# Performance work log

Measured on AMD Instinct MI355X. Metric: run time of the kernel, lower is better.

## Reference

```python
import jax, jax.numpy as jnp
import numpy as np

NUM_BINS = 30
MIN_BW = 1e-3
MIN_BH = 1e-3
MIN_D = 1e-3
LO_IN, HI_IN = 0.0, 1.0
LO_OUT, HI_OUT = 0.0, 1.0
DERIV_OUT_LO = (HI_OUT - LO_OUT) / (HI_IN - LO_IN)  # default outside derivatives
DERIV_OUT_HI = DERIV_OUT_LO
EPS = 1e-6
B, V = 65536, 64


def _cumparams(unnorm, lo, hi, min_size):
    # softmax bin sizes with a floor, cumsum into knot positions. [V,K] -> ([V,K+1],[V,K])
    K = unnorm.shape[-1]
    p = jax.nn.softmax(unnorm, axis=-1)
    p = min_size + (1.0 - min_size * K) * p
    cp = jnp.cumsum(p, axis=-1)
    cp = jnp.pad(cp, [(0, 0), (1, 0)])
    cp = (hi - lo) * cp + lo
    cp = cp.at[..., 0].set(lo).at[..., -1].set(hi)
    sizes = cp[..., 1:] - cp[..., :-1]
    return cp, sizes


def setup_inputs() -> dict:
    key = jax.random.key(0)
    k0, k1, k2, k3 = jax.random.split(key, 4)
    return {
        "inputs": jax.random.uniform(k0, (B, V), dtype=jnp.float32),
        "unnormalized_widths": jax.random.uniform(k1, (V, NUM_BINS), dtype=jnp.float32),
        "unnormalized_heights": jax.random.uniform(k2, (V, NUM_BINS), dtype=jnp.float32),
        "unnormalized_derivatives": jax.random.uniform(k3, (V, NUM_BINS - 1), dtype=jnp.float32),
    }


def reference(inputs, unnormalized_widths, unnormalized_heights, unnormalized_derivatives):
    K = NUM_BINS
    nb, nv = inputs.shape

    cumw, widths = _cumparams(unnormalized_widths, LO_IN, HI_IN, MIN_BW)      # [V,K+1],[V,K]
    cumh, heights = _cumparams(unnormalized_heights, LO_OUT, HI_OUT, MIN_BH)  # [V,K+1],[V,K]

    # boundary derivatives pinned so softplus(const)+MIN_D == 1
    const = float(np.log(np.exp(1.0 - MIN_D) - 1.0))
    ud = jnp.pad(unnormalized_derivatives, [(0, 0), (1, 1)], constant_values=const)
    derivs = MIN_D + jax.nn.softplus(ud)  # [V,K+1]
    delta = heights / widths              # [V,K]

    # per-element bin search (forward mode -> search in cumwidths)
    bounds = cumw.at[..., -1].add(EPS)                                   # [V,K+1]
    bin_idx = jnp.sum(inputs[..., None] >= bounds[None], axis=-1) - 1    # [B,V]
    bin_idx = jnp.clip(bin_idx, 0, K - 1)

    vidx = jnp.arange(nv)[None, :]  # broadcast variable index [1,V]
    icw = cumw[vidx, bin_idx]       # input_cumwidths [B,V]
    ibw = widths[vidx, bin_idx]
    ich = cumh[vidx, bin_idx]
    idl = delta[vidx, bin_idx]
    d0 = derivs[vidx, bin_idx]
    d1 = derivs[vidx, bin_idx + 1]
    ih = heights[vidx, bin_idx]

    theta = (inputs - icw) / ibw
    t1mt = theta * (1.0 - theta)
    numerator = ih * (idl * theta * theta + d0 * t1mt)
    denominator = idl + (d0 + d1 - 2.0 * idl) * t1mt
    spline_out = ich + numerator / denominator
    deriv_num = idl * idl * (d1 * theta * theta + 2.0 * idl * t1mt + d0 * (1.0 - theta) ** 2)
    spline_lad = jnp.log(deriv_num) - 2.0 * jnp.log(denominator)

    below = inputs < LO_IN
    above = inputs > HI_IN
    inside = ~(below | above)
    out_lo = LO_OUT + (inputs - LO_IN) * DERIV_OUT_LO
    out_hi = HI_OUT + (inputs - HI_IN) * DERIV_OUT_HI
    outputs = jnp.where(below, out_lo, jnp.where(above, out_hi, spline_out))
    logabsdet = jnp.where(inside, spline_lad, 0.0)
    return outputs, logabsdet
```

## Files before the change

kernel.cpp:

```cpp
#include <hip/hip_runtime.h>
#include <math.h>


#define NB 65536
#define NV 64
#define NKB 30
#define ROWF 153
#define OFF_B 0
#define OFF_W 32
#define OFF_C 62
#define OFF_H 92
#define OFF_D 122
#define NBLK 1024

__global__ __launch_bounds__(64) void rqs_params(const float* __restrict__ uw,
                                                 const float* __restrict__ uh,
                                                 const float* __restrict__ ud,
                                                 float* __restrict__ P) {
  const int v = blockIdx.x;
  const int lane = threadIdx.x;
  float* p = P + v * ROWF;
  const float MINB = 1e-3f;
  const float scale = 1.0f - MINB * (float)NKB;

  {
    float u = (lane < NKB) ? uw[v * NKB + lane] : -1e30f;
    float m = u;
#pragma unroll
    for (int s = 32; s >= 1; s >>= 1) m = fmaxf(m, __shfl_xor(m, s));
    float e = (lane < NKB) ? expf(u - m) : 0.0f;
    float t = e;
#pragma unroll
    for (int s = 32; s >= 1; s >>= 1) t += __shfl_xor(t, s);
    float pk = (lane < NKB) ? (MINB + scale * (e / t)) : 0.0f;
    float ci = pk;
#pragma unroll
    for (int s = 1; s < 64; s <<= 1) {
      float z = __shfl_up(ci, s);
      if (lane >= s) ci += z;
    }
    float ce = ci - pk;
    float nxt = (lane == NKB - 1) ? 1.0f : ci;
    if (lane < NKB) {
      p[OFF_B + lane + 1] = nxt;
      p[OFF_W + lane] = 1.0f / (nxt - ce);
    }
    if (lane == 0) p[OFF_B + 0] = 0.0f;
    if (lane == NKB) p[OFF_B + NKB] = 1.0f + 1e-6f;
    if (lane == NKB + 1) p[OFF_B + NKB + 1] = 3.0e38f;
  }
  {
    float u = (lane < NKB) ? uh[v * NKB + lane] : -1e30f;
    float m = u;
#pragma unroll
    for (int s = 32; s >= 1; s >>= 1) m = fmaxf(m, __shfl_xor(m, s));
    float e = (lane < NKB) ? expf(u - m) : 0.0f;
    float t = e;
#pragma unroll
    for (int s = 32; s >= 1; s >>= 1) t += __shfl_xor(t, s);
    float pk = (lane < NKB) ? (MINB + scale * (e / t)) : 0.0f;
    float ci = pk;
#pragma unroll
    for (int s = 1; s < 64; s <<= 1) {
      float z = __shfl_up(ci, s);
      if (lane >= s) ci += z;
    }
    float ce = ci - pk;
    float nxt = (lane == NKB - 1) ? 1.0f : ci;
    if (lane < NKB) {
      p[OFF_C + lane] = ce;
      p[OFF_H + lane] = nxt - ce;
    }
  }
  {
    const float CST = (float)log(exp(1.0 - 1e-3) - 1.0);
    if (lane <= NKB) {
      float x = (lane == 0 || lane == NKB) ? CST : ud[v * (NKB - 1) + lane - 1];
      float sp = (x > 0.f) ? (x + log1pf(expf(-x))) : log1pf(expf(x));
      p[OFF_D + lane] = 1e-3f + sp;
    }
  }
}

__global__ __launch_bounds__(256, 4) void rqs_main(const float* __restrict__ x,
                                                   const float* __restrict__ P,
                                                   float* __restrict__ out) {
  __shared__ float lds[NV * ROWF];
  {
    const float4* src = (const float4*)P;
    float4* dst = (float4*)lds;
    for (int i = threadIdx.x; i < (NV * ROWF) / 4; i += 256) dst[i] = src[i];
  }
  __syncthreads();

  const int N = NB * NV;
  const int n4 = N / 4;
  for (int gid = blockIdx.x * 256 + threadIdx.x; gid < n4; gid += NBLK * 256) {
    float4 xv = ((const float4*)x)[gid];
    int v0 = (gid & 15) * 4;

    float xs[4] = {xv.x, xv.y, xv.z, xv.w};
    float o[4], l[4];
#pragma unroll
    for (int j = 0; j < 4; ++j) {
      float xx = xs[j];
      const float* row = lds + (v0 + j) * ROWF;
      int idx = 0;
#pragma unroll
      for (int s = 16; s >= 1; s >>= 1) {
        int c = idx + s;
        idx = (xx >= row[OFF_B + c]) ? c : idx;
      }
      int b = idx > 29 ? 29 : idx;

      float icw  = row[OFF_B + b];
      float winv = row[OFF_W + b];
      float ich  = row[OFF_C + b];
      float ih   = row[OFF_H + b];
      float d0   = row[OFF_D + b];
      float d1   = row[OFF_D + b + 1];
      float idl  = ih * winv;

      float th   = (xx - icw) * winv;
      float omt  = 1.0f - th;
      float t1mt = th * omt;
      float th2  = th * th;
      float num  = ih * (idl * th2 + d0 * t1mt);
      float den  = idl + (d0 + d1 - 2.0f * idl) * t1mt;
      float rden = __frcp_rn(den);
      float so   = ich + num * rden;
      float dn   = idl * idl * (d1 * th2 + 2.0f * idl * t1mt + d0 * omt * omt);
      float sl   = __logf(dn * rden * rden);

      bool inside = !(xx < 0.0f) && !(xx > 1.0f);
      o[j] = inside ? so : xx;
      l[j] = inside ? sl : 0.0f;
    }
    float4 ov = {o[0], o[1], o[2], o[3]};
    float4 lv = {l[0], l[1], l[2], l[3]};
    ((float4*)out)[gid] = ov;
    ((float4*)(out + N))[gid] = lv;
  }
}

extern "C" void kernel_launch(void* const* d_in, const int* in_sizes, int n_in,
                              void* d_out, int out_size, void* d_ws, size_t ws_size,
                              hipStream_t stream) {
  const float* x  = (const float*)d_in[0];
  const float* uw = (const float*)d_in[1];
  const float* uh = (const float*)d_in[2];
  const float* ud = (const float*)d_in[3];
  float* out = (float*)d_out;
  float* P   = (float*)d_ws;

  rqs_params<<<NV, 64, 0, stream>>>(uw, uh, ud, P);
  rqs_main<<<NBLK, 256, 0, stream>>>(x, P, out);
}
```

Baseline: 92.01 us.

## Fuse parameter kernel into main kernel, recomputing spline tables per block in LDS

Drops the separate parameter-precompute kernel and its global workspace round trip. Each block now computes the softmax/cumsum/softplus tables for all 64 variables itself, with each of its 4 waves handling 16 variables, and writes them straight into shared memory. This removes one kernel launch and the dependency between the two kernels. In exchange, every one of the 1024 blocks repeats the table computation serially, which adds transcendental work and shuffle latency to each block's prologue.

After: 125.2 us. 36.0% more time.

```diff
diff --git a/kernel.cpp b/kernel.cpp
--- a/kernel.cpp
+++ b/kernel.cpp
@@ -13,83 +13,76 @@
 #define OFF_D 122
 #define NBLK 1024
 
-__global__ __launch_bounds__(64) void rqs_params(const float* __restrict__ uw,
-                                                 const float* __restrict__ uh,
-                                                 const float* __restrict__ ud,
-                                                 float* __restrict__ P) {
-  const int v = blockIdx.x;
-  const int lane = threadIdx.x;
-  float* p = P + v * ROWF;
+__global__ __launch_bounds__(256, 4) void rqs_fused(const float* __restrict__ x,
+                                                    const float* __restrict__ uw,
+                                                    const float* __restrict__ uh,
+                                                    const float* __restrict__ ud,
+                                                    float* __restrict__ out) {
+  __shared__ float lds[NV * ROWF];
+  const int lane = threadIdx.x & 63;
+  const int wave = threadIdx.x >> 6;
   const float MINB = 1e-3f;
   const float scale = 1.0f - MINB * (float)NKB;
 
-  {
-    float u = (lane < NKB) ? uw[v * NKB + lane] : -1e30f;
-    float m = u;
+  for (int t = 0; t < 16; ++t) {
+    const int v = wave * 16 + t;
+    float* p = lds + v * ROWF;
+
+    {
+      float u = (lane < NKB) ? uw[v * NKB + lane] : -1e30f;
+      float m = u;
 #pragma unroll
-    for (int s = 32; s >= 1; s >>= 1) m = fmaxf(m, __shfl_xor(m, s));
-    float e = (lane < NKB) ? expf(u - m) : 0.0f;
-    float t = e;
+      for (int s = 32; s >= 1; s >>= 1) m = fmaxf(m, __shfl_xor(m, s));
+      float e = (lane < NKB) ? expf(u - m) : 0.0f;
+      float tt = e;
 #pragma unroll
-    for (int s = 32; s >= 1; s >>= 1) t += __shfl_xor(t, s);
-    float pk = (lane < NKB) ? (MINB + scale * (e / t)) : 0.0f;
-    float ci = pk;
+      for (int s = 32; s >= 1; s >>= 1) tt += __shfl_xor(tt, s);
+      float pk = (lane < NKB) ? (MINB + scale * (e / tt)) : 0.0f;
+      float ci = pk;
 #pragma unroll
-    for (int s = 1; s < 64; s <<= 1) {
-      float z = __shfl_up(ci, s);
-      if (lane >= s) ci += z;
+      for (int s = 1; s < 64; s <<= 1) {
+        float z = __shfl_up(ci, s);
+        if (lane >= s) ci += z;
+      }
+      float ce = ci - pk;
+      float nxt = (lane == NKB - 1) ? 1.0f : ci;
+      if (lane < NKB - 1) p[OFF_B + lane + 1] = nxt;
+      if (lane < NKB) p[OFF_W + lane] = 1.0f / (nxt - ce);
+      if (lane == 0) p[OFF_B + 0] = 0.0f;
+      if (lane == NKB) p[OFF_B + NKB] = 1.0f + 1e-6f;
+      if (lane == NKB + 1) p[OFF_B + NKB + 1] = 3.0e38f;
     }
-    float ce = ci - pk;
-    float nxt = (lane == NKB - 1) ? 1.0f : ci;
-    if (lane < NKB) {
-      p[OFF_B + lane + 1] = nxt;
-      p[OFF_W + lane] = 1.0f / (nxt - ce);
+    {
+      float u = (lane < NKB) ? uh[v * NKB + lane] : -1e30f;
+      float m = u;
+#pragma unroll
+      for (int s = 32; s >= 1; s >>= 1) m = fmaxf(m, __shfl_xor(m, s));
+      float e = (lane < NKB) ? expf(u - m) : 0.0f;
+      float tt = e;
+#pragma unroll
+      for (int s = 32; s >= 1; s >>= 1) tt += __shfl_xor(tt, s);
+      float pk = (lane < NKB) ? (MINB + scale * (e / tt)) : 0.0f;
+      float ci = pk;
+#pragma unroll
+      for (int s = 1; s < 64; s <<= 1) {
+        float z = __shfl_up(ci, s);
+        if (lane >= s) ci += z;
+      }
+      float ce = ci - pk;
+      float nxt = (lane == NKB - 1) ? 1.0f : ci;
+      if (lane < NKB) {
+        p[OFF_C + lane] = ce;
+        p[OFF_H + lane] = nxt - ce;
+      }
     }
-    if (lane == 0) p[OFF_B + 0] = 0.0f;
-    if (lane == NKB) p[OFF_B + NKB] = 1.0f + 1e-6f;
-    if (lane == NKB + 1) p[OFF_B + NKB + 1] = 3.0e38f;
-  }
-  {
-    float u = (lane < NKB) ? uh[v * NKB + lane] : -1e30f;
-    float m = u;
-#pragma unroll
-    for (int s = 32; s >= 1; s >>= 1) m = fmaxf(m, __shfl_xor(m, s));
-    float e = (lane < NKB) ? expf(u - m) : 0.0f;
-    float t = e;
-#pragma unroll
-    for (int s = 32; s >= 1; s >>= 1) t += __shfl_xor(t, s);
-    float pk = (lane < NKB) ? (MINB + scale * (e / t)) : 0.0f;
-    float ci = pk;
-#pragma unroll
-    for (int s = 1; s < 64; s <<= 1) {
-      float z = __shfl_up(ci, s);
-      if (lane >= s) ci += z;
+    {
+      const float CST = (float)log(exp(1.0 - 1e-3) - 1.0);
+      if (lane <= NKB) {
+        float xv = (lane == 0 || lane == NKB) ? CST : ud[v * (NKB - 1) + lane - 1];
+        float sp = (xv > 0.f) ? (xv + log1pf(expf(-xv))) : log1pf(expf(xv));
+        p[OFF_D + lane] = 1e-3f + sp;
+      }
     }
-    float ce = ci - pk;
-    float nxt = (lane == NKB - 1) ? 1.0f : ci;
-    if (lane < NKB) {
-      p[OFF_C + lane] = ce;
-      p[OFF_H + lane] = nxt - ce;
-    }
-  }
-  {
-    const float CST = (float)log(exp(1.0 - 1e-3) - 1.0);
-    if (lane <= NKB) {
-      float x = (lane == 0 || lane == NKB) ? CST : ud[v * (NKB - 1) + lane - 1];
-      float sp = (x > 0.f) ? (x + log1pf(expf(-x))) : log1pf(expf(x));
-      p[OFF_D + lane] = 1e-3f + sp;
-    }
-  }
-}
-
-__global__ __launch_bounds__(256, 4) void rqs_main(const float* __restrict__ x,
-                                                   const float* __restrict__ P,
-                                                   float* __restrict__ out) {
-  __shared__ float lds[NV * ROWF];
-  {
-    const float4* src = (const float4*)P;
-    float4* dst = (float4*)lds;
-    for (int i = threadIdx.x; i < (NV * ROWF) / 4; i += 256) dst[i] = src[i];
   }
   __syncthreads();
 
@@ -151,8 +144,6 @@
   const float* uh = (const float*)d_in[2];
   const float* ud = (const float*)d_in[3];
   float* out = (float*)d_out;
-  float* P   = (float*)d_ws;
 
-  rqs_params<<<NV, 64, 0, stream>>>(uw, uh, ud, P);
-  rqs_main<<<NBLK, 256, 0, stream>>>(x, P, out);
+  rqs_fused<<<NBLK, 256, 0, stream>>>(x, uw, uh, ud, out);
 }
```

## Replace dependent binary bin search with two-level parallel count search

Applied to the files above, without the earlier changes.

Replaces the 5-step dependent binary search over knot positions with a two-level search. It loads 7 coarse knots per element, counts how many are exceeded to pick a group of 4, then loads 3 fine knots and counts again. Loads are batched across the 4 elements so LDS latency overlaps instead of chaining. It also swaps the correctly rounded reciprocal for the raw hardware rcp, and the params kernel stops writing knot 30 from lane 29 (lane 30 writes it instead). The change does more LDS reads per element in exchange for fewer serial load-compare steps, and may raise register pressure.

After: 93.29 us. No clear change (+1.4%).

```diff
diff --git a/kernel.cpp b/kernel.cpp
--- a/kernel.cpp
+++ b/kernel.cpp
@@ -41,10 +41,8 @@
     }
     float ce = ci - pk;
     float nxt = (lane == NKB - 1) ? 1.0f : ci;
-    if (lane < NKB) {
-      p[OFF_B + lane + 1] = nxt;
-      p[OFF_W + lane] = 1.0f / (nxt - ce);
-    }
+    if (lane < NKB - 1) p[OFF_B + lane + 1] = nxt;
+    if (lane < NKB) p[OFF_W + lane] = 1.0f / (nxt - ce);
     if (lane == 0) p[OFF_B + 0] = 0.0f;
     if (lane == NKB) p[OFF_B + NKB] = 1.0f + 1e-6f;
     if (lane == NKB + 1) p[OFF_B + NKB + 1] = 3.0e38f;
@@ -97,41 +95,66 @@
   const int n4 = N / 4;
   for (int gid = blockIdx.x * 256 + threadIdx.x; gid < n4; gid += NBLK * 256) {
     float4 xv = ((const float4*)x)[gid];
-    int v0 = (gid & 15) * 4;
+    const int v0 = (gid & 15) * 4;
+    float xs[4] = {xv.x, xv.y, xv.z, xv.w};
+    const float* rows[4];
+#pragma unroll
+    for (int j = 0; j < 4; ++j) rows[j] = lds + (v0 + j) * ROWF;
 
-    float xs[4] = {xv.x, xv.y, xv.z, xv.w};
+    float pA[4][7];
+#pragma unroll
+    for (int j = 0; j < 4; ++j)
+#pragma unroll
+      for (int i = 0; i < 7; ++i) pA[j][i] = rows[j][OFF_B + 4 * (i + 1)];
+    int base[4];
+#pragma unroll
+    for (int j = 0; j < 4; ++j) {
+      int c = 0;
+#pragma unroll
+      for (int i = 0; i < 7; ++i) c += (xs[j] >= pA[j][i]) ? 4 : 0;
+      base[j] = c;
+    }
+    float pB[4][3];
+#pragma unroll
+    for (int j = 0; j < 4; ++j)
+#pragma unroll
+      for (int t = 0; t < 3; ++t) pB[j][t] = rows[j][OFF_B + base[j] + t + 1];
+    int bb[4];
+#pragma unroll
+    for (int j = 0; j < 4; ++j) {
+      int m = 0;
+#pragma unroll
+      for (int t = 0; t < 3; ++t) m += (xs[j] >= pB[j][t]) ? 1 : 0;
+      int b = base[j] + m;
+      bb[j] = b > 29 ? 29 : b;
+    }
+    float icw[4], winv[4], ich[4], ih[4], d0[4], d1[4];
+#pragma unroll
+    for (int j = 0; j < 4; ++j) {
+      const float* r = rows[j];
+      const int b = bb[j];
+      icw[j]  = r[OFF_B + b];
+      winv[j] = r[OFF_W + b];
+      ich[j]  = r[OFF_C + b];
+      ih[j]   = r[OFF_H + b];
+      d0[j]   = r[OFF_D + b];
+      d1[j]   = r[OFF_D + b + 1];
+    }
     float o[4], l[4];
 #pragma unroll
     for (int j = 0; j < 4; ++j) {
-      float xx = xs[j];
-      const float* row = lds + (v0 + j) * ROWF;
-      int idx = 0;
-#pragma unroll
-      for (int s = 16; s >= 1; s >>= 1) {
-        int c = idx + s;
-        idx = (xx >= row[OFF_B + c]) ? c : idx;
-      }
-      int b = idx > 29 ? 29 : idx;
-
-      float icw  = row[OFF_B + b];
-      float winv = row[OFF_W + b];
-      float ich  = row[OFF_C + b];
-      float ih   = row[OFF_H + b];
-      float d0   = row[OFF_D + b];
-      float d1   = row[OFF_D + b + 1];
-      float idl  = ih * winv;
-
-      float th   = (xx - icw) * winv;
+      float xx   = xs[j];
+      float idl  = ih[j] * winv[j];
+      float th   = (xx - icw[j]) * winv[j];
       float omt  = 1.0f - th;
       float t1mt = th * omt;
       float th2  = th * th;
-      float num  = ih * (idl * th2 + d0 * t1mt);
-      float den  = idl + (d0 + d1 - 2.0f * idl) * t1mt;
-      float rden = __frcp_rn(den);
-      float so   = ich + num * rden;
-      float dn   = idl * idl * (d1 * th2 + 2.0f * idl * t1mt + d0 * omt * omt);
+      float num  = ih[j] * (idl * th2 + d0[j] * t1mt);
+      float den  = idl + (d0[j] + d1[j] - 2.0f * idl) * t1mt;
+      float rden = __builtin_amdgcn_rcpf(den);
+      float so   = ich[j] + num * rden;
+      float dn   = idl * idl * (d1[j] * th2 + 2.0f * idl * t1mt + d0[j] * omt * omt);
       float sl   = __logf(dn * rden * rden);
-
       bool inside = !(xx < 0.0f) && !(xx > 1.0f);
       o[j] = inside ? so : xx;
       l[j] = inside ? sl : 0.0f;
```

## Use 512-thread blocks with two prefetched float4 loads per thread

Applied to the files above, without the earlier changes.

Raises the block size to 512 and replaces the grid-stride loop with a fixed two-iteration body. Both input float4 loads are issued up front, before any compute, to raise memory-level parallelism. The reciprocal changes from round-to-nearest to the hardware rcp builtin. The params kernel also stops writing the last knot from the cumsum, because that slot is overwritten by the pinned boundary value. Together these cut loop overhead and aim to hide global load latency, at the cost of hardcoding the grid to cover exactly N/4 elements in two passes.

Result: no change. 90.87 us (-1.2%).

```diff
diff --git a/kernel.cpp b/kernel.cpp
--- a/kernel.cpp
+++ b/kernel.cpp
@@ -12,6 +12,7 @@
 #define OFF_H 92
 #define OFF_D 122
 #define NBLK 1024
+#define BSZ 512
 
 __global__ __launch_bounds__(64) void rqs_params(const float* __restrict__ uw,
                                                  const float* __restrict__ uh,
@@ -41,10 +42,8 @@
     }
     float ce = ci - pk;
     float nxt = (lane == NKB - 1) ? 1.0f : ci;
-    if (lane < NKB) {
-      p[OFF_B + lane + 1] = nxt;
-      p[OFF_W + lane] = 1.0f / (nxt - ce);
-    }
+    if (lane < NKB - 1) p[OFF_B + lane + 1] = nxt;
+    if (lane < NKB) p[OFF_W + lane] = 1.0f / (nxt - ce);
     if (lane == 0) p[OFF_B + 0] = 0.0f;
     if (lane == NKB) p[OFF_B + NKB] = 1.0f + 1e-6f;
     if (lane == NKB + 1) p[OFF_B + NKB + 1] = 3.0e38f;
@@ -82,65 +81,78 @@
   }
 }
 
-__global__ __launch_bounds__(256, 4) void rqs_main(const float* __restrict__ x,
+__device__ __forceinline__ void rqs_eval(const float* __restrict__ lds,
+                                         float4 xv, int v0,
+                                         float4* __restrict__ outp,
+                                         float4* __restrict__ ladp) {
+  float xs[4] = {xv.x, xv.y, xv.z, xv.w};
+  float o[4], l[4];
+#pragma unroll
+  for (int j = 0; j < 4; ++j) {
+    float xx = xs[j];
+    const float* row = lds + (v0 + j) * ROWF;
+    int idx = 0;
+#pragma unroll
+    for (int s = 16; s >= 1; s >>= 1) {
+      int c = idx + s;
+      idx = (xx >= row[OFF_B + c]) ? c : idx;
+    }
+    int b = idx > 29 ? 29 : idx;
+
+    float icw  = row[OFF_B + b];
+    float winv = row[OFF_W + b];
+    float ich  = row[OFF_C + b];
+    float ih   = row[OFF_H + b];
+    float d0   = row[OFF_D + b];
+    float d1   = row[OFF_D + b + 1];
+    float idl  = ih * winv;
+
+    float th   = (xx - icw) * winv;
+    float omt  = 1.0f - th;
+    float t1mt = th * omt;
+    float th2  = th * th;
+    float num  = ih * (idl * th2 + d0 * t1mt);
+    float den  = idl + (d0 + d1 - 2.0f * idl) * t1mt;
+    float rden = __builtin_amdgcn_rcpf(den);
+    float so   = ich + num * rden;
+    float dn   = idl * idl * (d1 * th2 + 2.0f * idl * t1mt + d0 * omt * omt);
+    float sl   = __logf(dn * rden * rden);
+
+    bool inside = !(xx < 0.0f) && !(xx > 1.0f);
+    o[j] = inside ? so : xx;
+    l[j] = inside ? sl : 0.0f;
+  }
+  *outp = (float4){o[0], o[1], o[2], o[3]};
+  *ladp = (float4){l[0], l[1], l[2], l[3]};
+}
+
+__global__ __launch_bounds__(BSZ, 8) void rqs_main(const float* __restrict__ x,
                                                    const float* __restrict__ P,
                                                    float* __restrict__ out) {
   __shared__ float lds[NV * ROWF];
   {
     const float4* src = (const float4*)P;
     float4* dst = (float4*)lds;
-    for (int i = threadIdx.x; i < (NV * ROWF) / 4; i += 256) dst[i] = src[i];
+    for (int i = threadIdx.x; i < (NV * ROWF) / 4; i += BSZ) dst[i] = src[i];
   }
   __syncthreads();
 
   const int N = NB * NV;
-  const int n4 = N / 4;
-  for (int gid = blockIdx.x * 256 + threadIdx.x; gid < n4; gid += NBLK * 256) {
-    float4 xv = ((const float4*)x)[gid];
-    int v0 = (gid & 15) * 4;
+  const int stride = NBLK * BSZ;
+  const int g0 = blockIdx.x * BSZ + threadIdx.x;
+  const int g1 = g0 + stride;
 
-    float xs[4] = {xv.x, xv.y, xv.z, xv.w};
-    float o[4], l[4];
-#pragma unroll
-    for (int j = 0; j < 4; ++j) {
-      float xx = xs[j];
-      const float* row = lds + (v0 + j) * ROWF;
-      int idx = 0;
-#pragma unroll
-      for (int s = 16; s >= 1; s >>= 1) {
-        int c = idx + s;
-        idx = (xx >= row[OFF_B + c]) ? c : idx;
-      }
-      int b = idx > 29 ? 29 : idx;
+  float4 xv0 = ((const float4*)x)[g0];
+  float4 xv1 = ((const float4*)x)[g1];
+  const int v0 = (g0 & 15) * 4;
 
-      float icw  = row[OFF_B + b];
-      float winv = row[OFF_W + b];
-      float ich  = row[OFF_C + b];
-      float ih   = row[OFF_H + b];
-      float d0   = row[OFF_D + b];
-      float d1   = row[OFF_D + b + 1];
-      float idl  = ih * winv;
-
-      float th   = (xx - icw) * winv;
-      float omt  = 1.0f - th;
-      float t1mt = th * omt;
-      float th2  = th * th;
-      float num  = ih * (idl * th2 + d0 * t1mt);
-      float den  = idl + (d0 + d1 - 2.0f * idl) * t1mt;
-      float rden = __frcp_rn(den);
-      float so   = ich + num * rden;
-      float dn   = idl * idl * (d1 * th2 + 2.0f * idl * t1mt + d0 * omt * omt);
-      float sl   = __logf(dn * rden * rden);
-
-      bool inside = !(xx < 0.0f) && !(xx > 1.0f);
-      o[j] = inside ? so : xx;
-      l[j] = inside ? sl : 0.0f;
-    }
-    float4 ov = {o[0], o[1], o[2], o[3]};
-    float4 lv = {l[0], l[1], l[2], l[3]};
-    ((float4*)out)[gid] = ov;
-    ((float4*)(out + N))[gid] = lv;
-  }
+  float4 ov, lv;
+  rqs_eval(lds, xv0, v0, &ov, &lv);
+  ((float4*)out)[g0] = ov;
+  ((float4*)(out + N))[g0] = lv;
+  rqs_eval(lds, xv1, v0, &ov, &lv);
+  ((float4*)out)[g1] = ov;
+  ((float4*)(out + N))[g1] = lv;
 }
 
 extern "C" void kernel_launch(void* const* d_in, const int* in_sizes, int n_in,
@@ -154,5 +166,5 @@
   float* P   = (float*)d_ws;
 
   rqs_params<<<NV, 64, 0, stream>>>(uw, uh, ud, P);
-  rqs_main<<<NBLK, 256, 0, stream>>>(x, P, out);
+  rqs_main<<<NBLK, BSZ, 0, stream>>>(x, P, out);
 }
```
